# Kernel tuning notes

Hardware: AMD Instinct MI355X
Metric: run time of the kernel (lower is better)

## Reference

```python
import jax, jax.numpy as jnp
import numpy as np

EMBED = 768
DIM = 800          # embed + 32 gender features
IN_C = 1024
GRID = 32          # img_size // patch_size(=1)
LN_EPS = 1e-5      # torch nn.LayerNorm default


def setup_inputs() -> dict:
    key = jax.random.key(0)
    ks = jax.random.split(key, 8)
    B = 32
    x = jax.random.normal(ks[0], (B, IN_C, GRID, GRID), dtype=jnp.float32)
    gender_encode = jax.random.normal(ks[1], (B, 32), dtype=jnp.float32)
    # PatchEmbed 1x1 conv (acts as per-pixel linear) + LayerNorm params
    conv_w = jax.random.normal(ks[2], (EMBED, IN_C), dtype=jnp.float32) * (IN_C ** -0.5)
    conv_b = jnp.zeros((EMBED,), dtype=jnp.float32)
    ln_g = jnp.ones((EMBED,), dtype=jnp.float32)
    ln_b = jnp.zeros((EMBED,), dtype=jnp.float32)
    cls_token = jax.random.normal(ks[3], (1, 1, EMBED), dtype=jnp.float32) * 0.02
    # Attention qkv linear (bias=True); proj is never used in the forward path
    qkv_w = jax.random.normal(ks[4], (3 * DIM, DIM), dtype=jnp.float32) * (DIM ** -0.5)
    qkv_b = jnp.zeros((3 * DIM,), dtype=jnp.float32)
    return {
        "x": x, "gender_encode": gender_encode,
        "conv_w": conv_w, "conv_b": conv_b,
        "ln_g": ln_g, "ln_b": ln_b,
        "cls_token": cls_token,
        "qkv_w": qkv_w, "qkv_b": qkv_b,
    }


def _forward(x, gender_encode, conv_w, conv_b, ln_g, ln_b, cls_token, qkv_w, qkv_b):
    B = x.shape[0]
    # PatchEmbed: 1x1 conv stride 1 == per-pixel linear; flatten(2).transpose(1,2)
    p = jnp.einsum('bchw,oc->bhwo', x, conv_w) + conv_b        # [B,32,32,768]
    p = p.reshape(B, GRID * GRID, EMBED)                        # [B,1024,768]
    mu = jnp.mean(p, axis=-1, keepdims=True)
    var = jnp.mean((p - mu) ** 2, axis=-1, keepdims=True)
    p = (p - mu) * jax.lax.rsqrt(var + LN_EPS) * ln_g + ln_b
    # prepend cls token, concat broadcast gender features
    cls = jnp.broadcast_to(cls_token, (B, 1, EMBED))
    t = jnp.concatenate([cls, p], axis=1)                       # [B,1025,768]
    g = jnp.broadcast_to(gender_encode[:, None, :], (B, t.shape[1], 32))
    t = jnp.concatenate([t, g], axis=2)                         # [B,1025,800]
    # Attention (note: self.norm / proj / v are unused in the original forward)
    qkv = t @ qkv_w.T + qkv_b                                   # [B,1025,2400]
    q = qkv[..., 0:DIM]
    k = qkv[..., DIM:2 * DIM]
    scale = DIM ** -0.5
    # only the cls-query row is ever used -> compute just that row
    scores = jnp.einsum('bc,bnc->bn', q[:, 0], k) * scale       # [B,1025]
    attn_cls = jax.nn.softmax(scores[:, 1:], axis=-1)           # [B,1024]
    return attn_cls.reshape(B, 1, GRID, GRID)


def reference(x, gender_encode, conv_w, conv_b, ln_g, ln_b, cls_token, qkv_w, qkv_b):
    return _forward(x, gender_encode, conv_w, conv_b, ln_g, ln_b, cls_token, qkv_w, qkv_b)
```

## Files before the change

### kernel.cpp

```cpp
#include <hip/hip_runtime.h>
#include <hip/hip_bf16.h>

#define EMBED 768
#define DIMQ  800
#define INC   1024
#define NPIX  1024

typedef __bf16 bf16_t;
typedef __bf16 bf16x8 __attribute__((ext_vector_type(8)));
typedef __bf16 bf16x2 __attribute__((ext_vector_type(2)));
typedef float  f32x4  __attribute__((ext_vector_type(4)));

#define GLD_LDS(gp, lp) __builtin_amdgcn_global_load_lds( \
    (const __attribute__((address_space(1))) void*)(gp),  \
    (__attribute__((address_space(3))) void*)(lp), 16, 0, 0)

__global__ __launch_bounds__(256)
void k_prep(const float* __restrict__ w, bf16_t* __restrict__ cw,
            const float* __restrict__ qkv_w, const float* __restrict__ qkv_b,
            const float* __restrict__ cls, const float* __restrict__ gender,
            float* __restrict__ q0b) {
    const int bi = blockIdx.x;
    const int t  = threadIdx.x;
    if (bi < 200) {
        const int wv = t >> 6, tl = t & 63;
        const int i = bi * 4 + wv;
        const float* row = qkv_w + (size_t)i * DIMQ;
        float ps = 0.f;
        for (int j = tl; j < EMBED; j += 64) ps += row[j] * cls[j];
#pragma unroll
        for (int off = 1; off < 64; off <<= 1) ps += __shfl_xor(ps, off, 64);
        if (tl < 32) {
            float g = 0.f;
#pragma unroll
            for (int j = 0; j < 32; ++j) g += row[EMBED + j] * gender[tl * 32 + j];
            q0b[tl * DIMQ + i] = ps + g + qkv_b[i];
        }
    } else {
        const int i = (bi - 200) * 256 + t;
        const int n = i >> 10, k = i & 1023;
        const int s = (k >> 3) & 7;
        const int src_k = (k & ~63) | (((s ^ (n & 7)) & 7) << 3) | (k & 7);
        cw[i] = (bf16_t)w[(size_t)n * 1024 + src_k];
    }
}

__global__ __launch_bounds__(256)
void k_u(const float* __restrict__ qkv_w, const float* __restrict__ q0b,
         const float* __restrict__ ln_g, float* __restrict__ u) {
    __shared__ float q0s[DIMQ];
    __shared__ float sh[8][33];
    int t = threadIdx.x;
    int b  = blockIdx.x / 24;
    int j0 = (blockIdx.x % 24) * 32;
    for (int i = t; i < DIMQ; i += 256) q0s[i] = q0b[b * DIMQ + i];
    __syncthreads();
    int j_l = t & 31, os = t >> 5;
    const float* wk = qkv_w + (size_t)DIMQ * DIMQ;
    const float* wp = wk + (size_t)(os * 100) * DIMQ + j0 + j_l;
    float acc = 0.f;
#pragma unroll 4
    for (int i = 0; i < 100; ++i) acc += wp[(size_t)i * DIMQ] * q0s[os * 100 + i];
    sh[os][j_l] = acc;
    __syncthreads();
    if (t < 32) {
        float s = 0.f;
#pragma unroll
        for (int o = 0; o < 8; ++o) s += sh[o][t];
        u[b * EMBED + j0 + t] = s * ln_g[j0 + t];
    }
}

__global__ __launch_bounds__(256, 3)
void k_main(const float* __restrict__ x, const bf16_t* __restrict__ cw,
            const float* __restrict__ conv_b, const float* __restrict__ u,
            float* __restrict__ partial) {
    __shared__ __align__(1024) unsigned char smem[49152];

    const int tid = threadIdx.x;
    const int bi = blockIdx.x;
    const int x8 = bi & 7;
    const int s  = bi >> 3;
    const int nt = s % 6;
    const int mt = (s / 6) * 8 + x8;
    const int b  = mt >> 3;
    const int gm = mt * 128;
    const int gmm = gm & 1023;
    const int gn = nt * 128;

    const int wv = tid >> 6;
    const int l  = tid & 63;
    const int lr = l >> 3;
    const int lc = l & 7;

    const int col  = l & 15;
    const int quad = l >> 4;
    const int wm   = (wv >> 1) * 64;
    const int wn   = (wv & 1) * 64;

    bf16_t* A  = (bf16_t*)smem;
    bf16_t* B0 = (bf16_t*)(smem + 16384);
    bf16_t* B1 = (bf16_t*)(smem + 32768);

    const int m4 = (tid >> 3) * 4;
    const float* xsrc = x + ((size_t)(b * 1024 + (tid & 7) * 8) * 1024) + gmm + m4;

    f32x4 f4[8];
    f32x4 C[4][4] = {};

#define LOADX(tt) do {                                                      \
        _Pragma("unroll")                                                   \
        for (int kk = 0; kk < 8; ++kk)                                      \
            f4[kk] = *(const f32x4*)(xsrc + (size_t)((tt) * 64 + kk) * 1024); \
    } while (0)

#define WRITEA() do {                                        \
        _Pragma("unroll")                                                   \
        for (int mm = 0; mm < 4; ++mm) {                                    \
            bf16x8 w8;                                                      \
            _Pragma("unroll")                                               \
            for (int kk = 0; kk < 8; ++kk) w8[kk] = (bf16_t)f4[kk][mm];     \
            const int r  = m4 + mm;                                         \
            const int ss = (tid & 7) ^ (r & 7);                             \
            *(bf16x8*)(A + r * 64 + ss * 8) = w8;                           \
        }                                                                   \
    } while (0)

#define GLDB(tt, dst) do {                                                  \
        _Pragma("unroll")                                                   \
        for (int p = 0; p < 4; ++p) {                                       \
            const int r = p * 32 + wv * 8 + lr;                             \
            GLD_LDS(cw + (size_t)(gn + r) * 1024 + (tt) * 64 + lc * 8,      \
                    (dst) + (p * 32 + wv * 8) * 64);                        \
        }                                                                   \
    } while (0)

#define WAIT_VM0()  asm volatile("s_waitcnt vmcnt(0)" ::: "memory")
#define WAIT_LGKM0() asm volatile("s_waitcnt lgkmcnt(0)" ::: "memory")
#define SBAR() do { __builtin_amdgcn_sched_barrier(0);                      \
                    __builtin_amdgcn_s_barrier();                           \
                    __builtin_amdgcn_sched_barrier(0); } while (0)

    LOADX(0);
    GLDB(0, B0);
    GLDB(1, B1);
    WAIT_VM0();
    WRITEA();
    LOADX(1);
    WAIT_LGKM0();
    SBAR();

#pragma unroll 1
    for (int t = 0; t < 16; ++t) {
        bf16_t* Bb = (t & 1) ? B1 : B0;
#pragma unroll
        for (int ks = 0; ks < 2; ++ks) {
            bf16x8 af[4], bg[4];
#pragma unroll
            for (int mi = 0; mi < 4; ++mi) {
                const int r  = wm + mi * 16 + col;
                const int ph = (ks * 4 + quad) ^ (r & 7);
                af[mi] = *(const bf16x8*)(A + r * 64 + ph * 8);
            }
#pragma unroll
            for (int ni = 0; ni < 4; ++ni) {
                const int r  = wn + ni * 16 + col;
                const int ph = (ks * 4 + quad) ^ (r & 7);
                bg[ni] = *(const bf16x8*)(Bb + r * 64 + ph * 8);
            }
#pragma unroll
            for (int mi = 0; mi < 4; ++mi)
#pragma unroll
                for (int ni = 0; ni < 4; ++ni)
                    C[mi][ni] = __builtin_amdgcn_mfma_f32_16x16x32_bf16(af[mi], bg[ni], C[mi][ni], 0, 0, 0);
        }
        if (t == 15) break;
        SBAR();
        WAIT_VM0();
        WRITEA();
        if (t < 14) {
            GLDB(t + 2, Bb);
            LOADX(t + 2);
        }
        WAIT_LGKM0();
        SBAR();
    }
#undef LOADX
#undef WRITEA
#undef GLDB

    SBAR();
    float cb[4], uv[4];
#pragma unroll
    for (int ni = 0; ni < 4; ++ni) {
        const int og = gn + wn + ni * 16 + col;
        cb[ni] = conv_b[og];
        uv[ni] = u[b * EMBED + og];
    }
    float* part = (float*)smem;
#pragma unroll
    for (int mi = 0; mi < 4; ++mi)
#pragma unroll
        for (int r = 0; r < 4; ++r) {
            float a = 0.f, sq = 0.f, d = 0.f;
#pragma unroll
            for (int ni = 0; ni < 4; ++ni) {
                float v = C[mi][ni][r] + cb[ni];
                a += v; sq += v * v; d += v * uv[ni];
            }
#pragma unroll
            for (int off = 1; off < 16; off <<= 1) {
                a  += __shfl_xor(a, off, 64);
                sq += __shfl_xor(sq, off, 64);
                d  += __shfl_xor(d, off, 64);
            }
            if (col == 0) {
                const int row = wm + mi * 16 + quad * 4 + r;
                float* pp = part + ((wv & 1) * 128 + row) * 3;
                pp[0] = a; pp[1] = sq; pp[2] = d;
            }
        }
    __syncthreads();
    if (tid < 128) {
        const float* p0 = part + tid * 3;
        const float* p1 = part + (128 + tid) * 3;
        const size_t pix = (size_t)gm + tid;
        partial[(size_t)(0 * 6 + nt) * 32768 + pix] = p0[0] + p1[0];
        partial[(size_t)(1 * 6 + nt) * 32768 + pix] = p0[1] + p1[1];
        partial[(size_t)(2 * 6 + nt) * 32768 + pix] = p0[2] + p1[2];
    }
}

__global__ __launch_bounds__(1024)
void k_final(const float* __restrict__ partial, const float* __restrict__ u,
             float* __restrict__ out) {
    __shared__ float red[16];
    __shared__ float bc[3];
    const int b = blockIdx.x, t = threadIdx.x;
    const int lane = t & 63, wid = t >> 6;

    float pu = (t < EMBED) ? u[b * EMBED + t] : 0.f;
#pragma unroll
    for (int off = 1; off < 64; off <<= 1) pu += __shfl_xor(pu, off, 64);
    if (lane == 0) red[wid] = pu;
    __syncthreads();
    if (t == 0) { float s = 0.f; for (int i = 0; i < 16; ++i) s += red[i]; bc[0] = s; }
    __syncthreads();
    const float Su = bc[0];

    const size_t m = (size_t)b * 1024 + t;
    float S1 = 0.f, S2 = 0.f, S3 = 0.f;
#pragma unroll
    for (int nt = 0; nt < 6; ++nt) {
        S1 += partial[(size_t)(0 * 6 + nt) * 32768 + m];
        S2 += partial[(size_t)(1 * 6 + nt) * 32768 + m];
        S3 += partial[(size_t)(2 * 6 + nt) * 32768 + m];
    }
    const float mu  = S1 * (1.f / 768.f);
    const float var = S2 * (1.f / 768.f) - mu * mu;
    const float sc  = 0.035355339059327376f * (S3 - mu * Su) * rsqrtf(var + 1e-5f);

    float mx = sc;
#pragma unroll
    for (int off = 1; off < 64; off <<= 1) mx = fmaxf(mx, __shfl_xor(mx, off, 64));
    if (lane == 0) red[wid] = mx;
    __syncthreads();
    if (t == 0) { float mm = -1e30f; for (int i = 0; i < 16; ++i) mm = fmaxf(mm, red[i]); bc[1] = mm; }
    __syncthreads();
    const float e = __expf(sc - bc[1]);
    float ss = e;
#pragma unroll
    for (int off = 1; off < 64; off <<= 1) ss += __shfl_xor(ss, off, 64);
    __syncthreads();
    if (lane == 0) red[wid] = ss;
    __syncthreads();
    if (t == 0) { float s = 0.f; for (int i = 0; i < 16; ++i) s += red[i]; bc[2] = s; }
    __syncthreads();
    out[m] = e / bc[2];
}

extern "C" void kernel_launch(void* const* d_in, const int* in_sizes, int n_in,
                              void* d_out, int out_size, void* d_ws, size_t ws_size,
                              hipStream_t stream) {
    const float* x      = (const float*)d_in[0];
    const float* gender = (const float*)d_in[1];
    const float* conv_w = (const float*)d_in[2];
    const float* conv_b = (const float*)d_in[3];
    const float* ln_g   = (const float*)d_in[4];
    const float* cls    = (const float*)d_in[6];
    const float* qkv_w  = (const float*)d_in[7];
    const float* qkv_b  = (const float*)d_in[8];
    float* out = (float*)d_out;

    char* ws = (char*)d_ws;
    bf16_t* cw      = (bf16_t*)ws;
    float*  q0b     = (float*)(ws + 1572864);
    float*  u       = (float*)(ws + 1675264);
    float*  partial = (float*)(ws + 1773568);

    hipLaunchKernelGGL(k_prep,  dim3(3272),  dim3(256),  0, stream,
                       conv_w, cw, qkv_w, qkv_b, cls, gender, q0b);
    hipLaunchKernelGGL(k_u,     dim3(768),   dim3(256),  0, stream, qkv_w, q0b, ln_g, u);
    hipLaunchKernelGGL(k_main,  dim3(1536),  dim3(256),  0, stream, x, cw, conv_b, u, partial);
    hipLaunchKernelGGL(k_final, dim3(32),    dim3(1024), 0, stream, partial, u, out);
}
```

Baseline: 302.1 us.

## Load conv weight fragments directly to registers and double-buffer A tile in LDS

The B operand (converted conv weight) is no longer staged through LDS with global_load_lds. Each lane now reads its MFMA fragments straight from global memory into registers, prefetching one half-step ahead, and the swizzle in k_prep is dropped. The freed LDS holds a double-buffered A tile, which cuts the barriers per k-step from two to one and shrinks LDS use, possibly raising occupancy. The cost is uncoalesced 16-byte global reads of B repeated across the waves sharing the same columns, plus more register pressure.

```diff
diff --git a/kernel.cpp b/kernel.cpp
--- a/kernel.cpp
+++ b/kernel.cpp
@@ -10,10 +10,6 @@
 typedef __bf16 bf16x8 __attribute__((ext_vector_type(8)));
 typedef __bf16 bf16x2 __attribute__((ext_vector_type(2)));
 typedef float  f32x4  __attribute__((ext_vector_type(4)));
-
-#define GLD_LDS(gp, lp) __builtin_amdgcn_global_load_lds( \
-    (const __attribute__((address_space(1))) void*)(gp),  \
-    (__attribute__((address_space(3))) void*)(lp), 16, 0, 0)
 
 __global__ __launch_bounds__(256)
 void k_prep(const float* __restrict__ w, bf16_t* __restrict__ cw,
@@ -38,10 +34,7 @@
         }
     } else {
         const int i = (bi - 200) * 256 + t;
-        const int n = i >> 10, k = i & 1023;
-        const int s = (k >> 3) & 7;
-        const int src_k = (k & ~63) | (((s ^ (n & 7)) & 7) << 3) | (k & 7);
-        cw[i] = (bf16_t)w[(size_t)n * 1024 + src_k];
+        cw[i] = (bf16_t)w[i];
     }
 }
 
@@ -75,7 +68,7 @@
 void k_main(const float* __restrict__ x, const bf16_t* __restrict__ cw,
             const float* __restrict__ conv_b, const float* __restrict__ u,
             float* __restrict__ partial) {
-    __shared__ __align__(1024) unsigned char smem[49152];
+    __shared__ __align__(1024) unsigned char smem[32768 + 3072];
 
     const int tid = threadIdx.x;
     const int bi = blockIdx.x;
@@ -90,22 +83,21 @@
 
     const int wv = tid >> 6;
     const int l  = tid & 63;
-    const int lr = l >> 3;
-    const int lc = l & 7;
 
     const int col  = l & 15;
     const int quad = l >> 4;
     const int wm   = (wv >> 1) * 64;
     const int wn   = (wv & 1) * 64;
 
-    bf16_t* A  = (bf16_t*)smem;
-    bf16_t* B0 = (bf16_t*)(smem + 16384);
-    bf16_t* B1 = (bf16_t*)(smem + 32768);
+    bf16_t* A0 = (bf16_t*)smem;
+    bf16_t* A1 = (bf16_t*)(smem + 16384);
 
     const int m4 = (tid >> 3) * 4;
     const float* xsrc = x + ((size_t)(b * 1024 + (tid & 7) * 8) * 1024) + gmm + m4;
+    const bf16_t* bgp = cw + (size_t)(gn + wn + col) * 1024 + quad * 8;
 
     f32x4 f4[8];
+    bf16x8 bgA[4], bgB[4];
     f32x4 C[4][4] = {};
 
 #define LOADX(tt) do {                                                      \
@@ -114,7 +106,7 @@
             f4[kk] = *(const f32x4*)(xsrc + (size_t)((tt) * 64 + kk) * 1024); \
     } while (0)
 
-#define WRITEA() do {                                        \
+#define WRITEA(dst) do {                                                    \
         _Pragma("unroll")                                                   \
         for (int mm = 0; mm < 4; ++mm) {                                    \
             bf16x8 w8;                                                      \
@@ -122,74 +114,58 @@
             for (int kk = 0; kk < 8; ++kk) w8[kk] = (bf16_t)f4[kk][mm];     \
             const int r  = m4 + mm;                                         \
             const int ss = (tid & 7) ^ (r & 7);                             \
-            *(bf16x8*)(A + r * 64 + ss * 8) = w8;                           \
+            *(bf16x8*)((dst) + r * 64 + ss * 8) = w8;                       \
         }                                                                   \
     } while (0)
 
-#define GLDB(tt, dst) do {                                                  \
-        _Pragma("unroll")                                                   \
-        for (int p = 0; p < 4; ++p) {                                       \
-            const int r = p * 32 + wv * 8 + lr;                             \
-            GLD_LDS(cw + (size_t)(gn + r) * 1024 + (tt) * 64 + lc * 8,      \
-                    (dst) + (p * 32 + wv * 8) * 64);                        \
+#define LOADBG(dst, tt, kss) do {                                           \
+        _Pragma("unroll")                                                   \
+        for (int ni = 0; ni < 4; ++ni)                                      \
+            dst[ni] = *(const bf16x8*)(bgp + (size_t)(ni * 16) * 1024       \
+                                       + (tt) * 64 + (kss) * 32);           \
+    } while (0)
+
+#define MFMA_HALF(kss, Ar, bg) do {                                         \
+        bf16x8 af[4];                                                       \
+        _Pragma("unroll")                                                   \
+        for (int mi = 0; mi < 4; ++mi) {                                    \
+            const int r  = wm + mi * 16 + col;                              \
+            const int ph = ((kss) * 4 + quad) ^ (r & 7);                    \
+            af[mi] = *(const bf16x8*)((Ar) + r * 64 + ph * 8);              \
         }                                                                   \
-    } while (0)
-
-#define WAIT_VM0()  asm volatile("s_waitcnt vmcnt(0)" ::: "memory")
-#define WAIT_LGKM0() asm volatile("s_waitcnt lgkmcnt(0)" ::: "memory")
-#define SBAR() do { __builtin_amdgcn_sched_barrier(0);                      \
-                    __builtin_amdgcn_s_barrier();                           \
-                    __builtin_amdgcn_sched_barrier(0); } while (0)
+        _Pragma("unroll")                                                   \
+        for (int mi = 0; mi < 4; ++mi)                                      \
+            _Pragma("unroll")                                               \
+            for (int ni = 0; ni < 4; ++ni)                                  \
+                C[mi][ni] = __builtin_amdgcn_mfma_f32_16x16x32_bf16(        \
+                    af[mi], bg[ni], C[mi][ni], 0, 0, 0);                    \
+    } while (0)
 
     LOADX(0);
-    GLDB(0, B0);
-    GLDB(1, B1);
-    WAIT_VM0();
-    WRITEA();
+    LOADBG(bgA, 0, 0);
+    WRITEA(A0);
     LOADX(1);
-    WAIT_LGKM0();
-    SBAR();
+    asm volatile("s_waitcnt lgkmcnt(0)" ::: "memory");
+    __builtin_amdgcn_s_barrier();
 
 #pragma unroll 1
     for (int t = 0; t < 16; ++t) {
-        bf16_t* Bb = (t & 1) ? B1 : B0;
-#pragma unroll
-        for (int ks = 0; ks < 2; ++ks) {
-            bf16x8 af[4], bg[4];
-#pragma unroll
-            for (int mi = 0; mi < 4; ++mi) {
-                const int r  = wm + mi * 16 + col;
-                const int ph = (ks * 4 + quad) ^ (r & 7);
-                af[mi] = *(const bf16x8*)(A + r * 64 + ph * 8);
-            }
-#pragma unroll
-            for (int ni = 0; ni < 4; ++ni) {
-                const int r  = wn + ni * 16 + col;
-                const int ph = (ks * 4 + quad) ^ (r & 7);
-                bg[ni] = *(const bf16x8*)(Bb + r * 64 + ph * 8);
-            }
-#pragma unroll
-            for (int mi = 0; mi < 4; ++mi)
-#pragma unroll
-                for (int ni = 0; ni < 4; ++ni)
-                    C[mi][ni] = __builtin_amdgcn_mfma_f32_16x16x32_bf16(af[mi], bg[ni], C[mi][ni], 0, 0, 0);
-        }
-        if (t == 15) break;
-        SBAR();
-        WAIT_VM0();
-        WRITEA();
-        if (t < 14) {
-            GLDB(t + 2, Bb);
-            LOADX(t + 2);
-        }
-        WAIT_LGKM0();
-        SBAR();
+        bf16_t* Ar = (t & 1) ? A1 : A0;
+        bf16_t* Aw = (t & 1) ? A0 : A1;
+        if (t + 1 < 16) WRITEA(Aw);
+        if (t + 2 < 16) LOADX(t + 2);
+        LOADBG(bgB, t, 1);
+        MFMA_HALF(0, Ar, bgA);
+        if (t + 1 < 16) LOADBG(bgA, t + 1, 0);
+        MFMA_HALF(1, Ar, bgB);
+        asm volatile("s_waitcnt lgkmcnt(0)" ::: "memory");
+        __builtin_amdgcn_s_barrier();
     }
 #undef LOADX
 #undef WRITEA
-#undef GLDB
-
-    SBAR();
+#undef LOADBG
+#undef MFMA_HALF
+
     float cb[4], uv[4];
 #pragma unroll
     for (int ni = 0; ni < 4; ++ni) {
@@ -197,7 +173,7 @@
         cb[ni] = conv_b[og];
         uv[ni] = u[b * EMBED + og];
     }
-    float* part = (float*)smem;
+    float* part = (float*)(smem + 32768);
 #pragma unroll
     for (int mi = 0; mi < 4; ++mi)
 #pragma unroll
```

New measurement: 370.8 us. +22.7%, slower.
